# Kernel optimization log

Measured on AMD Instinct MI355X. Metric: run time of the kernel, lower is better.

The kernel has to match this reference:

```python
import jax, jax.numpy as jnp
import numpy as np
import math

D_MODEL = 1024
N_HEADS = 16
D_K = 64
D_V = 64
B = 4
S = 1024


def setup_inputs() -> dict:
    key = jax.random.key(0)
    ks = jax.random.split(key, 11)
    # xavier-ish init scale for projections
    s_in = 1.0 / math.sqrt(D_MODEL)
    return {
        "queries": jax.random.normal(ks[0], (B, S, D_MODEL), jnp.float32),
        "keys": jax.random.normal(ks[1], (B, S, D_MODEL), jnp.float32),
        "values": jax.random.normal(ks[2], (B, S, D_MODEL), jnp.float32),
        "Wq": jax.random.normal(ks[3], (D_MODEL, N_HEADS * D_K), jnp.float32) * s_in,
        "bq": jnp.zeros((N_HEADS * D_K,), jnp.float32),
        "Wk": jax.random.normal(ks[4], (D_MODEL, N_HEADS * D_K), jnp.float32) * s_in,
        "bk": jnp.zeros((N_HEADS * D_K,), jnp.float32),
        "Wv": jax.random.normal(ks[5], (D_MODEL, N_HEADS * D_V), jnp.float32) * s_in,
        "bv": jnp.zeros((N_HEADS * D_V,), jnp.float32),
        "Wo": jax.random.normal(ks[6], (N_HEADS * D_V, D_MODEL), jnp.float32) * (1.0 / math.sqrt(N_HEADS * D_V)),
        "bo": jnp.zeros((D_MODEL,), jnp.float32),
    }


def reference(queries, keys, values, Wq, bq, Wk, bk, Wv, bv, Wo, bo):
    Bq, Sq, _ = queries.shape
    Sk = keys.shape[1]
    scale = 1.0 / math.sqrt(D_K)
    # projections -> [B, S, H, d]
    q = (queries @ Wq + bq).reshape(Bq, Sq, N_HEADS, D_K)
    k = (keys @ Wk + bk).reshape(Bq, Sk, N_HEADS, D_K)
    v = (values @ Wv + bv).reshape(Bq, Sk, N_HEADS, D_V)
    # scaled dot-product attention: scores [B, H, Sq, Sk]
    scores = jnp.einsum("bqhd,bkhd->bhqk", q, k) * scale
    attn = jax.nn.softmax(scores, axis=-1)
    # weighted values -> [B, Sq, H*D_V]
    out = jnp.einsum("bhqk,bkhd->bqhd", attn, v).reshape(Bq, Sq, N_HEADS * D_V)
    return out @ Wo + bo
```

## Files before the change

### kernel.cpp

```cpp
#include <hip/hip_runtime.h>
#include <hip/hip_bf16.h>

typedef __attribute__((ext_vector_type(4))) float f32x4;
typedef __attribute__((ext_vector_type(16))) float f32x16;
typedef __attribute__((ext_vector_type(8))) short bf16x8;
typedef __attribute__((ext_vector_type(4))) unsigned short u16x4;
typedef __attribute__((ext_vector_type(8))) unsigned short u16x8;
typedef __attribute__((ext_vector_type(2))) unsigned int u32x2;

#define MFMA16(a, b, c) __builtin_amdgcn_mfma_f32_16x16x32_bf16((a), (b), (c), 0, 0, 0)
#define MFMA32(a, b, c) __builtin_amdgcn_mfma_f32_32x32x16_bf16((a), (b), (c), 0, 0, 0)

static __device__ __forceinline__ unsigned short f2bf(float f) {
    union { float f; unsigned int u; } v; v.f = f;
    unsigned int r = v.u + 0x7FFFu + ((v.u >> 16) & 1u);
    return (unsigned short)(r >> 16);
}
static __device__ __forceinline__ unsigned int pk2(float x, float y) {
    unsigned int r;
    asm("v_cvt_pk_bf16_f32 %0, %1, %2" : "=v"(r) : "v"(x), "v"(y));
    return r;
}

static __device__ __forceinline__ void gload_lds16(const void* g, void* l) {
    __builtin_amdgcn_global_load_lds(
        (const __attribute__((address_space(1))) void*)g,
        (__attribute__((address_space(3))) void*)l, 16, 0, 0);
}

__global__ __launch_bounds__(256) void prepass(
    const float* __restrict__ q, const float* __restrict__ k,
    const float* __restrict__ v, const float* __restrict__ Wq,
    const float* __restrict__ Wk, const float* __restrict__ Wv,
    const float* __restrict__ Wo, unsigned short* __restrict__ qc,
    unsigned short* __restrict__ kc, unsigned short* __restrict__ vc,
    unsigned short* __restrict__ Wt, unsigned short* __restrict__ Wot) {
    __shared__ unsigned short T[64][65];
    const int id = blockIdx.x, t = threadIdx.x;
    if (id < 6144) {
        const int z = id >> 11;
        const float* src = z == 0 ? q : (z == 1 ? k : v);
        unsigned short* dst = z == 0 ? qc : (z == 1 ? kc : vc);
        size_t off = ((size_t)(id & 2047) * 256 + t) * 8;
        f32x4 a = *(const f32x4*)&src[off];
        f32x4 b = *(const f32x4*)&src[off + 4];
        union { unsigned int u[4]; u16x8 v; } o;
        o.u[0] = pk2(a[0], a[1]); o.u[1] = pk2(a[2], a[3]);
        o.u[2] = pk2(b[0], b[1]); o.u[3] = pk2(b[2], b[3]);
        *(u16x8*)&dst[off] = o.v;
    } else {
        int r = id - 6144;
        const int z = r >> 8; r &= 255;
        const float* W = z == 0 ? Wq : (z == 1 ? Wk : (z == 2 ? Wv : Wo));
        unsigned short* Wd = z < 3 ? (Wt + (size_t)z * 1024 * 1024) : Wot;
        const int k0 = (r >> 4) * 64, n0 = (r & 15) * 64;
        const int rl = t >> 4, c4 = (t & 15) * 4;
#pragma unroll
        for (int i = 0; i < 4; ++i) {
            f32x4 vv = *(const f32x4*)&W[(size_t)(k0 + rl + 16 * i) * 1024 + n0 + c4];
#pragma unroll
            for (int j = 0; j < 4; ++j) T[rl + 16 * i][c4 + j] = f2bf(vv[j]);
        }
        __syncthreads();
#pragma unroll
        for (int i = 0; i < 4; ++i) {
            u16x4 o;
#pragma unroll
            for (int j = 0; j < 4; ++j) o[j] = T[c4 + j][rl + 16 * i];
            *(u16x4*)&Wd[(size_t)(n0 + rl + 16 * i) * 1024 + k0 + c4] = o;
        }
    }
}

template <bool OUT_BF16, int BM, int BN, int SWZ, int MINW>
__global__ __launch_bounds__(256, MINW) void gemm_fast(
    const unsigned short* __restrict__ A0, const unsigned short* __restrict__ A1,
    const unsigned short* __restrict__ A2, const unsigned short* __restrict__ Wt,
    const float* __restrict__ b0, const float* __restrict__ b1,
    const float* __restrict__ b2, void* __restrict__ Outv, int ldo) {
    constexpr int MF = BM / 32;
    constexpr int NF = BN / 32;
    __shared__ __align__(16) unsigned short As[2][BM * 32];
    __shared__ __align__(16) unsigned short Bs[2][BN * 32];

    const int t = threadIdx.x;
    const int w = t >> 6, lane = t & 63;
    const int wr = w >> 1, wc = w & 1;
    const int g = lane >> 4, r15 = lane & 15;

    const int id = blockIdx.x;
    int bm, bn;
    if (SWZ == 0) {
        const int xcd = id & 7, local = id >> 3;
        const int half = local >= 48 ? 1 : 0;
        const int ww = local - half * 48;
        const int gg = xcd * 2 + half;
        bm = ((gg >> 2) * 8 + (ww & 7)) * BM;
        bn = ((gg & 3) * 6 + (ww >> 3)) * BN;
    } else {
        const int xcd = id & 7, local = id >> 3;
        bm = (xcd * 8 + (local & 7)) * BM;
        bn = (local >> 3) * BN;
    }
    const int msel = bn >> 10;
    const unsigned short* A = msel == 0 ? A0 : (msel == 1 ? A1 : A2);
    const float* bias = msel == 0 ? b0 : (msel == 1 ? b1 : b2);
    const int l4 = lane >> 2, c8 = (lane & 3) * 8;

    f32x4 acc[MF][NF];
#pragma unroll
    for (int m = 0; m < MF; ++m)
#pragma unroll
        for (int n = 0; n < NF; ++n) acc[m][n] = (f32x4){0.f, 0.f, 0.f, 0.f};

#define G_STAGE(BUF, KT)                                                          \
    {                                                                             \
        gload_lds16(&A[(size_t)(bm + 16 * w + l4) * 1024 + (KT) + c8],            \
                    &As[BUF][w * 512]);                                           \
        if (BM == 128)                                                            \
            gload_lds16(&A[(size_t)(bm + 16 * (w + 4) + l4) * 1024 + (KT) + c8],  \
                        &As[BUF][(w + 4) * 512]);                                 \
        gload_lds16(&Wt[(size_t)(bn + 16 * w + l4) * 1024 + (KT) + c8],           \
                    &Bs[BUF][w * 512]);                                           \
        if (BN == 128)                                                            \
            gload_lds16(&Wt[(size_t)(bn + 16 * (w + 4) + l4) * 1024 + (KT) + c8], \
                        &Bs[BUF][(w + 4) * 512]);                                 \
    }

    G_STAGE(0, 0);
    __syncthreads();

    int cur = 0;
    for (int kt = 0; kt < 1024; kt += 32) {
        if (kt < 992) G_STAGE(cur ^ 1, kt + 32);
        bf16x8 af[MF], bfr[NF];
#pragma unroll
        for (int m = 0; m < MF; ++m)
            af[m] = *(const bf16x8*)&As[cur][(wr * (BM / 2) + m * 16 + r15) * 32 + g * 8];
#pragma unroll
        for (int n = 0; n < NF; ++n)
            bfr[n] = *(const bf16x8*)&Bs[cur][(wc * (BN / 2) + n * 16 + r15) * 32 + g * 8];
        __builtin_amdgcn_s_setprio(1);
#pragma unroll
        for (int m = 0; m < MF; ++m)
#pragma unroll
            for (int n = 0; n < NF; ++n)
                acc[m][n] = MFMA16(af[m], bfr[n], acc[m][n]);
        __builtin_amdgcn_s_setprio(0);
        __syncthreads();
        cur ^= 1;
    }
#undef G_STAGE

    float* Of = (float*)Outv;
    unsigned short* Ob = (unsigned short*)Outv;
#pragma unroll
    for (int n = 0; n < NF; ++n) {
        int col = bn + wc * (BN / 2) + n * 16 + r15;
        float bv = bias[col & 1023];
#pragma unroll
        for (int m = 0; m < MF; ++m) {
#pragma unroll
            for (int r = 0; r < 4; ++r) {
                int row = bm + wr * (BM / 2) + m * 16 + g * 4 + r;
                float val = acc[m][n][r] + bv;
                if (OUT_BF16)
                    Ob[(size_t)row * ldo + col] = f2bf(val);
                else
                    Of[(size_t)row * ldo + col] = val;
            }
        }
    }
}

__global__ __launch_bounds__(256, 2) void attn32_kernel(
    const unsigned short* __restrict__ Q, const unsigned short* __restrict__ K,
    const unsigned short* __restrict__ V, unsigned short* __restrict__ O, int ld) {
    __shared__ __align__(16) unsigned short Kls[2][64 * 80];
    __shared__ __align__(16) unsigned short Vls[2][64 * 80];

    const int t = threadIdx.x;
    const int w = t >> 6, lane = t & 63;
    const int q5 = lane & 31, hi = lane >> 5;

    const int id = blockIdx.x;
    const int sid = (id & 7) * 64 + (id >> 3);
    const int bh = sid >> 3, qb = sid & 7;
    const int b = bh >> 4, h = bh & 15;
    const int brow = b * 1024;
    const int q0 = qb * 128;

    const float c2 = 0.18033688f;

    const unsigned short* Qrow = Q + (size_t)(brow + q0 + w * 32 + q5) * ld + h * 64;
    bf16x8 qreg[8];
#pragma unroll
    for (int j = 0; j < 8; ++j) qreg[j] = *(const bf16x8*)&Qrow[8 * j];
    bf16x8 qsel[4];
#pragma unroll
    for (int kk = 0; kk < 4; ++kk) qsel[kk] = hi ? qreg[2 * kk + 1] : qreg[2 * kk];

    const int krow = t >> 2, kpart = t & 3;
    const int vp = t & 31, vdc = t >> 5;
    const unsigned short* Kg = K + h * 64;
    const unsigned short* Vg = V + h * 64;

    u16x8 kr0, kr1, vr0, vr1;
#define STG_LOAD(KT)                                                            \
    {                                                                           \
        size_t kro = (size_t)(brow + (KT) + krow) * ld;                         \
        kr0 = *(const u16x8*)&Kg[kro + kpart * 8];                              \
        kr1 = *(const u16x8*)&Kg[kro + kpart * 8 + 32];                         \
        size_t vro = (size_t)(brow + (KT) + 2 * vp) * ld;                       \
        vr0 = *(const u16x8*)&Vg[vro + vdc * 8];                                \
        vr1 = *(const u16x8*)&Vg[vro + ld + vdc * 8];                           \
    }
#define STG_WRITE(BUF)                                                          \
    {                                                                           \
        char* kb_ = (char*)Kls[BUF];                                            \
        int tg_ = (krow & 7) << 4;                                              \
        *(u16x8*)(kb_ + krow * 160 + ((kpart * 16) ^ tg_)) = kr0;               \
        *(u16x8*)(kb_ + krow * 160 + (((kpart + 4) * 16) ^ tg_)) = kr1;         \
        char* vb_ = (char*)Vls[BUF];                                            \
        _Pragma("unroll") for (int j_ = 0; j_ < 8; ++j_) {                      \
            int d_ = vdc * 8 + j_;                                              \
            unsigned int pk_ = (unsigned int)(unsigned short)vr0[j_] |          \
                               ((unsigned int)(unsigned short)vr1[j_] << 16);   \
            *(unsigned int*)(vb_ + d_ * 160 + ((vp * 4) ^ ((d_ & 7) << 4)))     \
                = pk_;                                                          \
        }                                                                       \
    }

    f32x16 acc0 = {}, acc1 = {};
    float mrun = -1e30f, lrun = 0.f;

    STG_LOAD(0);
    STG_WRITE(0);
    __syncthreads();

    int cur = 0;
    for (int tile = 0; tile < 16; ++tile) {
        const bool more = tile < 15;
        if (more) STG_LOAD(tile * 64 + 64);

        char* kb = (char*)Kls[cur];
        f32x16 st0 = {}, st1 = {};
        {
            const int tg0 = (q5 & 7) << 4;
            char* kp0 = kb + q5 * 160;
            char* kp1 = kb + (q5 + 32) * 160;
            __builtin_amdgcn_s_setprio(1);
#pragma unroll
            for (int kk = 0; kk < 4; ++kk) {
                int so = ((2 * kk + hi) * 16) ^ tg0;
                bf16x8 kf0 = *(const bf16x8*)(kp0 + so);
                bf16x8 kf1 = *(const bf16x8*)(kp1 + so);
                st0 = MFMA32(kf0, qsel[kk], st0);
                st1 = MFMA32(kf1, qsel[kk], st1);
            }
            __builtin_amdgcn_s_setprio(0);
        }

        float mloc = fmaxf(st0[0], st0[1]);
#pragma unroll
        for (int r = 2; r < 16; ++r) mloc = fmaxf(mloc, st0[r]);
#pragma unroll
        for (int r = 0; r < 16; ++r) mloc = fmaxf(mloc, st1[r]);
        mloc = fmaxf(mloc, __shfl_xor(mloc, 32));
        if (!__all(mloc - mrun <= 64.f)) {
            float mnew = fmaxf(mrun, mloc);
            float sf = exp2f((mrun - mnew) * c2);
            mrun = mnew;
            lrun *= sf;
#pragma unroll
            for (int r = 0; r < 16; ++r) { acc0[r] *= sf; acc1[r] *= sf; }
        }
        float mneg = -mrun * c2;
        float rs = 0.f;
#pragma unroll
        for (int r = 0; r < 16; ++r) {
            st0[r] = exp2f(fmaf(st0[r], c2, mneg));
            rs += st0[r];
        }
#pragma unroll
        for (int r = 0; r < 16; ++r) {
            st1[r] = exp2f(fmaf(st1[r], c2, mneg));
            rs += st1[r];
        }
        rs += __shfl_xor(rs, 32);
        lrun += rs;

        char* vb = (char*)Vls[cur];
        const int tgv = (q5 & 7) << 4;
        char* vp0 = vb + q5 * 160;
        char* vp1 = vb + (q5 + 32) * 160;
        __builtin_amdgcn_s_setprio(1);
#define PV_HALF(ST, CT)                                                         \
    _Pragma("unroll") for (int ks = 0; ks < 2; ++ks) {                          \
        unsigned int a0 = pk2(ST[8 * ks + 0], ST[8 * ks + 1]);                  \
        unsigned int a1 = pk2(ST[8 * ks + 2], ST[8 * ks + 3]);                  \
        unsigned int a2 = pk2(ST[8 * ks + 4], ST[8 * ks + 5]);                  \
        unsigned int a3 = pk2(ST[8 * ks + 6], ST[8 * ks + 7]);                  \
        unsigned int x0 = __shfl_xor(a0, 32), x1 = __shfl_xor(a1, 32);          \
        unsigned int x2 = __shfl_xor(a2, 32), x3 = __shfl_xor(a3, 32);          \
        union { unsigned int u[4]; bf16x8 v; } pfu;                             \
        pfu.u[0] = hi ? x2 : a0;                                                \
        pfu.u[1] = hi ? x3 : a1;                                                \
        pfu.u[2] = hi ? a2 : x0;                                                \
        pfu.u[3] = hi ? a3 : x1;                                                \
        int co = ((32 * (2 * (CT) + ks) + 16 * hi)) ^ tgv;                      \
        bf16x8 vf0 = *(const bf16x8*)(vp0 + co);                                \
        bf16x8 vf1 = *(const bf16x8*)(vp1 + co);                                \
        acc0 = MFMA32(vf0, pfu.v, acc0);                                        \
        acc1 = MFMA32(vf1, pfu.v, acc1);                                        \
    }
        PV_HALF(st0, 0);
        PV_HALF(st1, 1);
        __builtin_amdgcn_s_setprio(0);

        if (more) STG_WRITE(cur ^ 1);
        __syncthreads();
        cur ^= 1;
    }

    const float inv = 1.0f / lrun;
    unsigned short* Orow = O + (size_t)(brow + q0 + w * 32 + q5) * 1024 + h * 64;
#pragma unroll
    for (int k = 0; k < 4; ++k) {
        int d0 = 8 * k + 4 * hi;
        u32x2 pa, pb;
        pa[0] = pk2(acc0[4 * k + 0] * inv, acc0[4 * k + 1] * inv);
        pa[1] = pk2(acc0[4 * k + 2] * inv, acc0[4 * k + 3] * inv);
        *(u32x2*)&Orow[d0] = pa;
        pb[0] = pk2(acc1[4 * k + 0] * inv, acc1[4 * k + 1] * inv);
        pb[1] = pk2(acc1[4 * k + 2] * inv, acc1[4 * k + 3] * inv);
        *(u32x2*)&Orow[32 + d0] = pb;
    }
#undef STG_LOAD
#undef STG_WRITE
#undef PV_HALF
}

extern "C" void kernel_launch(void* const* d_in, const int* in_sizes, int n_in,
                              void* d_out, int out_size, void* d_ws, size_t ws_size,
                              hipStream_t stream) {
    const float* q  = (const float*)d_in[0];
    const float* k  = (const float*)d_in[1];
    const float* v  = (const float*)d_in[2];
    const float* Wq = (const float*)d_in[3];
    const float* bq = (const float*)d_in[4];
    const float* Wk = (const float*)d_in[5];
    const float* bk = (const float*)d_in[6];
    const float* Wv = (const float*)d_in[7];
    const float* bv = (const float*)d_in[8];
    const float* Wo = (const float*)d_in[9];
    const float* bo = (const float*)d_in[10];

    const size_t M1 = (size_t)1024 * 1024;
    unsigned short* qc  = (unsigned short*)d_ws;
    unsigned short* kc  = qc + 4 * M1;
    unsigned short* vc  = kc + 4 * M1;
    unsigned short* Wt  = vc + 4 * M1;
    unsigned short* Wot = Wt + 3 * M1;
    unsigned short* QKV = Wot + M1;
    unsigned short* Ob  = qc;

    dim3 bt(256, 1, 1);
    prepass<<<dim3(7168), bt, 0, stream>>>(q, k, v, Wq, Wk, Wv, Wo,
                                           qc, kc, vc, Wt, Wot);
    gemm_fast<true, 128, 128, 0, 2><<<dim3(768), bt, 0, stream>>>(
        qc, kc, vc, Wt, bq, bk, bv, QKV, 3072);
    attn32_kernel<<<dim3(512), bt, 0, stream>>>(
        QKV, QKV + 1024, QKV + 2048, Ob, 3072);
    gemm_fast<false, 64, 64, 1, 4><<<dim3(1024), bt, 0, stream>>>(
        Ob, Ob, Ob, Wot, bo, bo, bo, d_out, 1024);
}
```

Baseline: 211.9 us.

## Fuse fp32-to-bf16 activation conversion into QKV GEMM and retile output GEMM

The separate prepass that converted the q/k/v activations to bf16 is removed. The QKV GEMM now loads fp32 activations straight into registers, converts them, and writes them to LDS, software-pipelined against the MFMA loop, which removes a full read-write round trip of the activation tensors. The output projection GEMM is changed from 64x64 to 128x64 tiles with a new XCD mapping and fewer blocks. The cost is more register pressure and VALU conversion work inside the GEMM, plus doubled A-side global traffic because fp32 is loaded instead of bf16.

```diff
diff --git a/kernel.cpp b/kernel.cpp
--- a/kernel.cpp
+++ b/kernel.cpp
@@ -28,60 +28,41 @@
         (__attribute__((address_space(3))) void*)l, 16, 0, 0);
 }
 
-__global__ __launch_bounds__(256) void prepass(
-    const float* __restrict__ q, const float* __restrict__ k,
-    const float* __restrict__ v, const float* __restrict__ Wq,
-    const float* __restrict__ Wk, const float* __restrict__ Wv,
-    const float* __restrict__ Wo, unsigned short* __restrict__ qc,
-    unsigned short* __restrict__ kc, unsigned short* __restrict__ vc,
+__global__ __launch_bounds__(256) void prepass_w(
+    const float* __restrict__ Wq, const float* __restrict__ Wk,
+    const float* __restrict__ Wv, const float* __restrict__ Wo,
     unsigned short* __restrict__ Wt, unsigned short* __restrict__ Wot) {
     __shared__ unsigned short T[64][65];
-    const int id = blockIdx.x, t = threadIdx.x;
-    if (id < 6144) {
-        const int z = id >> 11;
-        const float* src = z == 0 ? q : (z == 1 ? k : v);
-        unsigned short* dst = z == 0 ? qc : (z == 1 ? kc : vc);
-        size_t off = ((size_t)(id & 2047) * 256 + t) * 8;
-        f32x4 a = *(const f32x4*)&src[off];
-        f32x4 b = *(const f32x4*)&src[off + 4];
-        union { unsigned int u[4]; u16x8 v; } o;
-        o.u[0] = pk2(a[0], a[1]); o.u[1] = pk2(a[2], a[3]);
-        o.u[2] = pk2(b[0], b[1]); o.u[3] = pk2(b[2], b[3]);
-        *(u16x8*)&dst[off] = o.v;
-    } else {
-        int r = id - 6144;
-        const int z = r >> 8; r &= 255;
-        const float* W = z == 0 ? Wq : (z == 1 ? Wk : (z == 2 ? Wv : Wo));
-        unsigned short* Wd = z < 3 ? (Wt + (size_t)z * 1024 * 1024) : Wot;
-        const int k0 = (r >> 4) * 64, n0 = (r & 15) * 64;
-        const int rl = t >> 4, c4 = (t & 15) * 4;
-#pragma unroll
-        for (int i = 0; i < 4; ++i) {
-            f32x4 vv = *(const f32x4*)&W[(size_t)(k0 + rl + 16 * i) * 1024 + n0 + c4];
-#pragma unroll
-            for (int j = 0; j < 4; ++j) T[rl + 16 * i][c4 + j] = f2bf(vv[j]);
-        }
-        __syncthreads();
-#pragma unroll
-        for (int i = 0; i < 4; ++i) {
-            u16x4 o;
-#pragma unroll
-            for (int j = 0; j < 4; ++j) o[j] = T[c4 + j][rl + 16 * i];
-            *(u16x4*)&Wd[(size_t)(n0 + rl + 16 * i) * 1024 + k0 + c4] = o;
-        }
-    }
-}
-
-template <bool OUT_BF16, int BM, int BN, int SWZ, int MINW>
-__global__ __launch_bounds__(256, MINW) void gemm_fast(
-    const unsigned short* __restrict__ A0, const unsigned short* __restrict__ A1,
-    const unsigned short* __restrict__ A2, const unsigned short* __restrict__ Wt,
+    int r = blockIdx.x;
+    const int z = r >> 8; r &= 255;
+    const float* W = z == 0 ? Wq : (z == 1 ? Wk : (z == 2 ? Wv : Wo));
+    unsigned short* Wd = z < 3 ? (Wt + (size_t)z * 1024 * 1024) : Wot;
+    const int k0 = (r >> 4) * 64, n0 = (r & 15) * 64;
+    const int t = threadIdx.x;
+    const int rl = t >> 4, c4 = (t & 15) * 4;
+#pragma unroll
+    for (int i = 0; i < 4; ++i) {
+        f32x4 vv = *(const f32x4*)&W[(size_t)(k0 + rl + 16 * i) * 1024 + n0 + c4];
+#pragma unroll
+        for (int j = 0; j < 4; ++j) T[rl + 16 * i][c4 + j] = f2bf(vv[j]);
+    }
+    __syncthreads();
+#pragma unroll
+    for (int i = 0; i < 4; ++i) {
+        u16x4 o;
+#pragma unroll
+        for (int j = 0; j < 4; ++j) o[j] = T[c4 + j][rl + 16 * i];
+        *(u16x4*)&Wd[(size_t)(n0 + rl + 16 * i) * 1024 + k0 + c4] = o;
+    }
+}
+
+__global__ __launch_bounds__(256, 2) void gemm_qkv(
+    const float* __restrict__ A0, const float* __restrict__ A1,
+    const float* __restrict__ A2, const unsigned short* __restrict__ Wt,
     const float* __restrict__ b0, const float* __restrict__ b1,
-    const float* __restrict__ b2, void* __restrict__ Outv, int ldo) {
-    constexpr int MF = BM / 32;
-    constexpr int NF = BN / 32;
-    __shared__ __align__(16) unsigned short As[2][BM * 32];
-    __shared__ __align__(16) unsigned short Bs[2][BN * 32];
+    const float* __restrict__ b2, unsigned short* __restrict__ Out) {
+    __shared__ __align__(16) unsigned short As[2][128 * 32];
+    __shared__ __align__(16) unsigned short Bs[2][128 * 32];
 
     const int t = threadIdx.x;
     const int w = t >> 6, lane = t & 63;
@@ -89,23 +70,117 @@
     const int g = lane >> 4, r15 = lane & 15;
 
     const int id = blockIdx.x;
-    int bm, bn;
-    if (SWZ == 0) {
-        const int xcd = id & 7, local = id >> 3;
-        const int half = local >= 48 ? 1 : 0;
-        const int ww = local - half * 48;
-        const int gg = xcd * 2 + half;
-        bm = ((gg >> 2) * 8 + (ww & 7)) * BM;
-        bn = ((gg & 3) * 6 + (ww >> 3)) * BN;
-    } else {
-        const int xcd = id & 7, local = id >> 3;
-        bm = (xcd * 8 + (local & 7)) * BM;
-        bn = (local >> 3) * BN;
-    }
+    const int xcd = id & 7, local = id >> 3;
+    const int half = local >= 48 ? 1 : 0;
+    const int ww = local - half * 48;
+    const int gg = xcd * 2 + half;
+    const int bm = ((gg >> 2) * 8 + (ww & 7)) * 128;
+    const int bn = ((gg & 3) * 6 + (ww >> 3)) * 128;
+
     const int msel = bn >> 10;
-    const unsigned short* A = msel == 0 ? A0 : (msel == 1 ? A1 : A2);
+    const float* A = msel == 0 ? A0 : (msel == 1 ? A1 : A2);
     const float* bias = msel == 0 ? b0 : (msel == 1 ? b1 : b2);
     const int l4 = lane >> 2, c8 = (lane & 3) * 8;
+    const int rowA0 = bm + 16 * w + l4, rowA1 = bm + 16 * (w + 4) + l4;
+
+    f32x4 acc[4][4];
+#pragma unroll
+    for (int m = 0; m < 4; ++m)
+#pragma unroll
+        for (int n = 0; n < 4; ++n) acc[m][n] = (f32x4){0.f, 0.f, 0.f, 0.f};
+
+    f32x4 a0lo, a0hi, a1lo, a1hi;
+#define A_LOAD(KT)                                                              \
+    {                                                                           \
+        const float* p0 = &A[(size_t)rowA0 * 1024 + (KT) + c8];                 \
+        a0lo = *(const f32x4*)p0; a0hi = *(const f32x4*)(p0 + 4);               \
+        const float* p1 = &A[(size_t)rowA1 * 1024 + (KT) + c8];                 \
+        a1lo = *(const f32x4*)p1; a1hi = *(const f32x4*)(p1 + 4);               \
+    }
+#define A_WRITE(BUF)                                                            \
+    {                                                                           \
+        union { unsigned int u[4]; u16x8 v; } o_;                               \
+        o_.u[0] = pk2(a0lo[0], a0lo[1]); o_.u[1] = pk2(a0lo[2], a0lo[3]);       \
+        o_.u[2] = pk2(a0hi[0], a0hi[1]); o_.u[3] = pk2(a0hi[2], a0hi[3]);       \
+        *(u16x8*)&As[BUF][(16 * w + l4) * 32 + c8] = o_.v;                      \
+        o_.u[0] = pk2(a1lo[0], a1lo[1]); o_.u[1] = pk2(a1lo[2], a1lo[3]);       \
+        o_.u[2] = pk2(a1hi[0], a1hi[1]); o_.u[3] = pk2(a1hi[2], a1hi[3]);       \
+        *(u16x8*)&As[BUF][(16 * (w + 4) + l4) * 32 + c8] = o_.v;                \
+    }
+#define B_STAGE(BUF, KT)                                                        \
+    {                                                                           \
+        gload_lds16(&Wt[(size_t)(bn + 16 * w + l4) * 1024 + (KT) + c8],         \
+                    &Bs[BUF][w * 512]);                                         \
+        gload_lds16(&Wt[(size_t)(bn + 16 * (w + 4) + l4) * 1024 + (KT) + c8],   \
+                    &Bs[BUF][(w + 4) * 512]);                                   \
+    }
+
+    A_LOAD(0);
+    B_STAGE(0, 0);
+    A_WRITE(0);
+    __syncthreads();
+
+    int cur = 0;
+    for (int kt = 0; kt < 1024; kt += 32) {
+        if (kt < 992) {
+            A_LOAD(kt + 32);
+            B_STAGE(cur ^ 1, kt + 32);
+        }
+        bf16x8 af[4], bfr[4];
+#pragma unroll
+        for (int m = 0; m < 4; ++m)
+            af[m] = *(const bf16x8*)&As[cur][(wr * 64 + m * 16 + r15) * 32 + g * 8];
+#pragma unroll
+        for (int n = 0; n < 4; ++n)
+            bfr[n] = *(const bf16x8*)&Bs[cur][(wc * 64 + n * 16 + r15) * 32 + g * 8];
+        __builtin_amdgcn_s_setprio(1);
+#pragma unroll
+        for (int m = 0; m < 4; ++m)
+#pragma unroll
+            for (int n = 0; n < 4; ++n)
+                acc[m][n] = MFMA16(af[m], bfr[n], acc[m][n]);
+        __builtin_amdgcn_s_setprio(0);
+        if (kt < 992) A_WRITE(cur ^ 1);
+        __syncthreads();
+        cur ^= 1;
+    }
+#undef A_LOAD
+#undef A_WRITE
+#undef B_STAGE
+
+#pragma unroll
+    for (int n = 0; n < 4; ++n) {
+        int col = bn + wc * 64 + n * 16 + r15;
+        float bv = bias[col & 1023];
+#pragma unroll
+        for (int m = 0; m < 4; ++m) {
+#pragma unroll
+            for (int r = 0; r < 4; ++r) {
+                int row = bm + wr * 64 + m * 16 + g * 4 + r;
+                Out[(size_t)row * 3072 + col] = f2bf(acc[m][n][r] + bv);
+            }
+        }
+    }
+}
+
+__global__ __launch_bounds__(256, 2) void gemm_out(
+    const unsigned short* __restrict__ A, const unsigned short* __restrict__ Wt,
+    const float* __restrict__ bias, float* __restrict__ Out) {
+    constexpr int BM = 128, BN = 64, MF = 4, NF = 2;
+    __shared__ __align__(16) unsigned short As[2][BM * 32];
+    __shared__ __align__(16) unsigned short Bs[2][BN * 32];
+
+    const int t = threadIdx.x;
+    const int w = t >> 6, lane = t & 63;
+    const int wr = w >> 1, wc = w & 1;
+    const int g = lane >> 4, r15 = lane & 15;
+
+    constexpr int MPX = (4096 / BM) / 8;
+    const int id = blockIdx.x;
+    const int xcd = id & 7, local = id >> 3;
+    const int bm = (xcd * MPX + (local % MPX)) * BM;
+    const int bn = (local / MPX) * BN;
+    const int l4 = lane >> 2, c8 = (lane & 3) * 8;
 
     f32x4 acc[MF][NF];
 #pragma unroll
@@ -113,18 +188,14 @@
 #pragma unroll
         for (int n = 0; n < NF; ++n) acc[m][n] = (f32x4){0.f, 0.f, 0.f, 0.f};
 
-#define G_STAGE(BUF, KT)                                                          \
-    {                                                                             \
-        gload_lds16(&A[(size_t)(bm + 16 * w + l4) * 1024 + (KT) + c8],            \
-                    &As[BUF][w * 512]);                                           \
-        if (BM == 128)                                                            \
-            gload_lds16(&A[(size_t)(bm + 16 * (w + 4) + l4) * 1024 + (KT) + c8],  \
-                        &As[BUF][(w + 4) * 512]);                                 \
-        gload_lds16(&Wt[(size_t)(bn + 16 * w + l4) * 1024 + (KT) + c8],           \
-                    &Bs[BUF][w * 512]);                                           \
-        if (BN == 128)                                                            \
-            gload_lds16(&Wt[(size_t)(bn + 16 * (w + 4) + l4) * 1024 + (KT) + c8], \
-                        &Bs[BUF][(w + 4) * 512]);                                 \
+#define G_STAGE(BUF, KT)                                                        \
+    {                                                                           \
+        gload_lds16(&A[(size_t)(bm + 16 * w + l4) * 1024 + (KT) + c8],          \
+                    &As[BUF][w * 512]);                                         \
+        gload_lds16(&A[(size_t)(bm + 16 * (w + 4) + l4) * 1024 + (KT) + c8],    \
+                    &As[BUF][(w + 4) * 512]);                                   \
+        gload_lds16(&Wt[(size_t)(bn + 16 * w + l4) * 1024 + (KT) + c8],         \
+                    &Bs[BUF][(w * 512) % (BN * 32)]);                           \
     }
 
     G_STAGE(0, 0);
@@ -136,10 +207,10 @@
         bf16x8 af[MF], bfr[NF];
 #pragma unroll
         for (int m = 0; m < MF; ++m)
-            af[m] = *(const bf16x8*)&As[cur][(wr * (BM / 2) + m * 16 + r15) * 32 + g * 8];
+            af[m] = *(const bf16x8*)&As[cur][(wr * 64 + m * 16 + r15) * 32 + g * 8];
 #pragma unroll
         for (int n = 0; n < NF; ++n)
-            bfr[n] = *(const bf16x8*)&Bs[cur][(wc * (BN / 2) + n * 16 + r15) * 32 + g * 8];
+            bfr[n] = *(const bf16x8*)&Bs[cur][(wc * 32 + n * 16 + r15) * 32 + g * 8];
         __builtin_amdgcn_s_setprio(1);
 #pragma unroll
         for (int m = 0; m < MF; ++m)
@@ -152,22 +223,16 @@
     }
 #undef G_STAGE
 
-    float* Of = (float*)Outv;
-    unsigned short* Ob = (unsigned short*)Outv;
 #pragma unroll
     for (int n = 0; n < NF; ++n) {
-        int col = bn + wc * (BN / 2) + n * 16 + r15;
-        float bv = bias[col & 1023];
+        int col = bn + wc * 32 + n * 16 + r15;
+        float bv = bias[col];
 #pragma unroll
         for (int m = 0; m < MF; ++m) {
 #pragma unroll
             for (int r = 0; r < 4; ++r) {
-                int row = bm + wr * (BM / 2) + m * 16 + g * 4 + r;
-                float val = acc[m][n][r] + bv;
-                if (OUT_BF16)
-                    Ob[(size_t)row * ldo + col] = f2bf(val);
-                else
-                    Of[(size_t)row * ldo + col] = val;
+                int row = bm + wr * 64 + m * 16 + g * 4 + r;
+                Out[(size_t)row * 1024 + col] = acc[m][n][r] + bv;
             }
         }
     }
@@ -357,21 +422,15 @@
     const float* bo = (const float*)d_in[10];
 
     const size_t M1 = (size_t)1024 * 1024;
-    unsigned short* qc  = (unsigned short*)d_ws;
-    unsigned short* kc  = qc + 4 * M1;
-    unsigned short* vc  = kc + 4 * M1;
-    unsigned short* Wt  = vc + 4 * M1;
+    unsigned short* Wt  = (unsigned short*)d_ws;
     unsigned short* Wot = Wt + 3 * M1;
     unsigned short* QKV = Wot + M1;
-    unsigned short* Ob  = qc;
+    unsigned short* Ob  = QKV + 12 * M1;
 
     dim3 bt(256, 1, 1);
-    prepass<<<dim3(7168), bt, 0, stream>>>(q, k, v, Wq, Wk, Wv, Wo,
-                                           qc, kc, vc, Wt, Wot);
-    gemm_fast<true, 128, 128, 0, 2><<<dim3(768), bt, 0, stream>>>(
-        qc, kc, vc, Wt, bq, bk, bv, QKV, 3072);
+    prepass_w<<<dim3(1024), bt, 0, stream>>>(Wq, Wk, Wv, Wo, Wt, Wot);
+    gemm_qkv<<<dim3(768), bt, 0, stream>>>(q, k, v, Wt, bq, bk, bv, QKV);
     attn32_kernel<<<dim3(512), bt, 0, stream>>>(
         QKV, QKV + 1024, QKV + 2048, Ob, 3072);
-    gemm_fast<false, 64, 64, 1, 4><<<dim3(1024), bt, 0, stream>>>(
-        Ob, Ob, Ob, Wot, bo, bo, bo, d_out, 1024);
-}
+    gemm_out<<<dim3(512), bt, 0, stream>>>(Ob, Wot, bo, (float*)d_out);
+}
```

Measured after the change: 223.4 us. 1.05x slower.
